# Kernel tuning notes

Measured on AMD Instinct MI355X. Metric: run time of the kernel, lower is better.

## Reference

```python
import jax, jax.numpy as jnp
import numpy as np

NEG = -9e15  # kept for fidelity though mask is unused in original forward

def setup_inputs() -> dict:
    key = jax.random.key(0)
    k1, k2, k3 = jax.random.split(key, 3)
    N, Fin, Fout = 8192, 512, 256
    x = jax.random.normal(k1, (N, Fin), dtype=jnp.float32)
    # xavier_uniform with gain=1.414 ~ U(-b, b), b = gain*sqrt(6/(fan_in+fan_out))
    bW = 1.414 * np.sqrt(6.0 / (Fin + Fout))
    W = jax.random.uniform(k2, (Fin, Fout), minval=-bW, maxval=bW, dtype=jnp.float32)
    ba = 1.414 * np.sqrt(6.0 / (2 * Fout + 1))
    a = jax.random.uniform(k3, (2 * Fout, 1), minval=-ba, maxval=ba, dtype=jnp.float32)
    return {"x": x, "W": W, "a": a}

def reference(x, W, a):
    # h: [N, Fout]
    h = x @ W
    Fout = h.shape[1]
    # Algebraic decomposition of additive score: e_ij = relu(a1.h_i + a2.h_j)
    a1, a2 = a[:Fout, 0], a[Fout:, 0]  # [Fout], [Fout]
    f = h @ a1  # [N] contribution of row node i
    g = h @ a2  # [N] contribution of col node j
    e = jax.nn.relu(f[:, None] + g[None, :])  # [N, N]
    attention = jax.nn.softmax(e, axis=1)
    h_prime = attention @ h  # [N, Fout]
    return jax.nn.elu(h_prime)
```

## Files before the change

### kernel.cpp

```cpp
#include <hip/hip_runtime.h>
#include <math.h>

#define NROWS 8192
#define FIN   512
#define FOUT  256
#define NCHUNK 512
#define CHROWS 16

typedef _Float16 f16;
typedef _Float16 f16x8 __attribute__((ext_vector_type(8)));
typedef float    f32x4 __attribute__((ext_vector_type(4)));

__global__ __launch_bounds__(256) void prep_wt(const float* __restrict__ W,
                                               f16* __restrict__ Wt,
                                               float* __restrict__ fg) {
    const int n = blockIdx.x, t = threadIdx.x;
    Wt[(size_t)n * FIN + t]       = (f16)W[(size_t)t * FOUT + n];
    Wt[(size_t)n * FIN + t + 256] = (f16)W[(size_t)(t + 256) * FOUT + n];
    if (n < 64) fg[n * 256 + t] = 0.f;
}

__global__ __launch_bounds__(256) void gemm_fg(const float* __restrict__ x,
                                               const f16* __restrict__ Wt,
                                               const float* __restrict__ a,
                                               f16* __restrict__ h,
                                               float* __restrict__ f,
                                               float* __restrict__ g) {
    __shared__ __align__(16) f16 As[64][136];
    __shared__ __align__(16) f16 Bs[64][136];
    __shared__ float sf[2][64], sg[2][64];
    const int tid = threadIdx.x;
    const int n0 = blockIdx.x * 64;
    const int m0 = blockIdx.y * 64;
    const int srow = tid >> 2, sseg = (tid & 3) * 8;
    const int w = tid >> 6, lane = tid & 63;
    const int wm = (w & 1) * 32, wn = (w >> 1) * 32;
    const int l15 = lane & 15, quad = lane >> 4;

    float4 pa0[4], pa1[4];
    f16x8 pb[4];
#pragma unroll
    for (int j = 0; j < 4; ++j) {
        const float* xp = &x[(size_t)(m0 + srow) * FIN + j * 32 + sseg];
        pa0[j] = *(const float4*)xp;
        pa1[j] = *(const float4*)(xp + 4);
        pb[j] = *(const f16x8*)&Wt[(size_t)(n0 + srow) * FIN + j * 32 + sseg];
    }

    f32x4 acc[2][2] = {};
    for (int k0 = 0; k0 < FIN; k0 += 128) {
        __syncthreads();
#pragma unroll
        for (int j = 0; j < 4; ++j) {
            f16x8 t;
            t[0] = (f16)pa0[j].x; t[1] = (f16)pa0[j].y;
            t[2] = (f16)pa0[j].z; t[3] = (f16)pa0[j].w;
            t[4] = (f16)pa1[j].x; t[5] = (f16)pa1[j].y;
            t[6] = (f16)pa1[j].z; t[7] = (f16)pa1[j].w;
            *(f16x8*)&As[srow][j * 32 + sseg] = t;
            *(f16x8*)&Bs[srow][j * 32 + sseg] = pb[j];
        }
        __syncthreads();
        if (k0 + 128 < FIN) {
#pragma unroll
            for (int j = 0; j < 4; ++j) {
                const float* xp = &x[(size_t)(m0 + srow) * FIN + k0 + 128 + j * 32 + sseg];
                pa0[j] = *(const float4*)xp;
                pa1[j] = *(const float4*)(xp + 4);
                pb[j] = *(const f16x8*)&Wt[(size_t)(n0 + srow) * FIN + k0 + 128 + j * 32 + sseg];
            }
        }
#pragma unroll
        for (int kk = 0; kk < 4; ++kk) {
            f16x8 af[2], bf[2];
#pragma unroll
            for (int ti = 0; ti < 2; ++ti)
                af[ti] = *(const f16x8*)&As[wm + ti * 16 + l15][kk * 32 + quad * 8];
#pragma unroll
            for (int tj = 0; tj < 2; ++tj)
                bf[tj] = *(const f16x8*)&Bs[wn + tj * 16 + l15][kk * 32 + quad * 8];
#pragma unroll
            for (int ti = 0; ti < 2; ++ti)
#pragma unroll
                for (int tj = 0; tj < 2; ++tj)
                    acc[ti][tj] = __builtin_amdgcn_mfma_f32_16x16x32_f16(af[ti], bf[tj], acc[ti][tj], 0, 0, 0);
        }
    }
#pragma unroll
    for (int ti = 0; ti < 2; ++ti)
#pragma unroll
        for (int tj = 0; tj < 2; ++tj) {
            const int col = n0 + wn + tj * 16 + l15;
#pragma unroll
            for (int r = 0; r < 4; ++r) {
                const int row = m0 + wm + ti * 16 + quad * 4 + r;
                h[(size_t)row * FOUT + col] = (f16)acc[ti][tj][r];
            }
        }
    const float a1c0 = a[n0 + wn + l15];
    const float a1c1 = a[n0 + wn + 16 + l15];
    const float a2c0 = a[FOUT + n0 + wn + l15];
    const float a2c1 = a[FOUT + n0 + wn + 16 + l15];
    const int wnIdx = w >> 1;
#pragma unroll
    for (int ti = 0; ti < 2; ++ti) {
        float pf[4], pg[4];
#pragma unroll
        for (int r = 0; r < 4; ++r) {
            pf[r] = acc[ti][0][r] * a1c0 + acc[ti][1][r] * a1c1;
            pg[r] = acc[ti][0][r] * a2c0 + acc[ti][1][r] * a2c1;
        }
#pragma unroll
        for (int off = 8; off >= 1; off >>= 1)
#pragma unroll
            for (int r = 0; r < 4; ++r) {
                pf[r] += __shfl_xor(pf[r], off, 16);
                pg[r] += __shfl_xor(pg[r], off, 16);
            }
        if (l15 == 0)
#pragma unroll
            for (int r = 0; r < 4; ++r) {
                sf[wnIdx][wm + ti * 16 + quad * 4 + r] = pf[r];
                sg[wnIdx][wm + ti * 16 + quad * 4 + r] = pg[r];
            }
    }
    __syncthreads();
    if (tid < 64) {
        atomicAdd(&f[m0 + tid], sf[0][tid] + sf[1][tid]);
        atomicAdd(&g[m0 + tid], sg[0][tid] + sg[1][tid]);
    }
}

__global__ __launch_bounds__(256) void rank_scatter(const float* __restrict__ g,
                                                    float* __restrict__ gs,
                                                    int* __restrict__ perm) {
    const int t = threadIdx.x;
    const int jl = t & 31;
    const int seg = t >> 5;
    const int j = blockIdx.x * 32 + jl;
    const float gj = g[j];
    const int base = seg * (NROWS / 8);
    int cnt = 0;
    for (int r = 0; r < NROWS / 8; r += 4) {
        const float4 v = *(const float4*)&g[base + r];
        const int i0 = base + r;
        cnt += (v.x < gj) || (v.x == gj && (i0 + 0) < j);
        cnt += (v.y < gj) || (v.y == gj && (i0 + 1) < j);
        cnt += (v.z < gj) || (v.z == gj && (i0 + 2) < j);
        cnt += (v.w < gj) || (v.w == gj && (i0 + 3) < j);
    }
    __shared__ int part[8][32];
    part[seg][jl] = cnt;
    __syncthreads();
    if (seg == 0) {
        int rank = 0;
#pragma unroll
        for (int s = 0; s < 8; ++s) rank += part[s][jl];
        gs[rank] = gj;
        perm[rank] = j;
    }
}

__global__ __launch_bounds__(256) void scan_pass1(const f16* __restrict__ h,
                                                  const int* __restrict__ perm,
                                                  const float* __restrict__ gs,
                                                  const float* __restrict__ f,
                                                  float* __restrict__ c0,
                                                  float* __restrict__ c1,
                                                  float* __restrict__ c1s,
                                                  int* __restrict__ n0arr) {
    const int b = blockIdx.x, c = threadIdx.x;
    if (b < NCHUNK) {
        const int base = b * CHROWS;
        __shared__ int p[CHROWS];
        __shared__ float wl[CHROWS];
        if (c < CHROWS) {
            p[c] = perm[base + c];
            wl[c] = expf(gs[base + c] - gs[NROWS - 1]);
        }
        __syncthreads();
        float s0 = 0.f, s1 = 0.f;
        for (int r = 0; r < CHROWS; ++r) {
            float v = (float)h[(size_t)p[r] * FOUT + c];
            s0 += v;
            s1 += wl[r] * v;
        }
        c0[b * FOUT + c] = s0;
        c1[b * FOUT + c] = s1;
        if (c == 0) {
            float t = 0.f;
            for (int r = 0; r < CHROWS; ++r) t += wl[r];
            c1s[b] = t;
        }
    } else {
        const int i = (b - NCHUNK) * 256 + c;
        const float tt = -f[i];
        int lo = 0, hi = NROWS;
        while (lo < hi) {
            int mid = (lo + hi) >> 1;
            if (gs[mid] <= tt) lo = mid + 1; else hi = mid;
        }
        n0arr[i] = lo;
    }
}

__global__ __launch_bounds__(256) void scan_pass2(const float* __restrict__ c0,
                                                  const float* __restrict__ c1,
                                                  const float* __restrict__ c1s,
                                                  float* __restrict__ o0,
                                                  float* __restrict__ o1,
                                                  float* __restrict__ o1s) {
    const int b = blockIdx.x, t = threadIdx.x;
    __shared__ float sb[256];
    if (b < 256) {
        const float e0 = c0[(2 * t) * FOUT + b];
        const float e1 = c0[(2 * t + 1) * FOUT + b];
        const float local = e0 + e1;
        sb[t] = local;
        __syncthreads();
        for (int off = 1; off < 256; off <<= 1) {
            float add = (t >= off) ? sb[t - off] : 0.f;
            __syncthreads();
            sb[t] += add;
            __syncthreads();
        }
        const float ex = sb[t] - local;
        o0[(2 * t) * FOUT + b] = ex;
        o0[(2 * t + 1) * FOUT + b] = ex + e0;
    } else if (b < 512) {
        const int col = b - 256;
        const float e0 = c1[(2 * t) * FOUT + col];
        const float e1 = c1[(2 * t + 1) * FOUT + col];
        const float local = e0 + e1;
        sb[t] = local;
        __syncthreads();
        for (int off = 1; off < 256; off <<= 1) {
            float add = (t + off < 256) ? sb[t + off] : 0.f;
            __syncthreads();
            sb[t] += add;
            __syncthreads();
        }
        const float exs = sb[t] - local;
        o1[(2 * t) * FOUT + col] = exs + e1;
        o1[(2 * t + 1) * FOUT + col] = exs;
    } else {
        const float e0 = c1s[2 * t];
        const float e1 = c1s[2 * t + 1];
        const float local = e0 + e1;
        sb[t] = local;
        __syncthreads();
        for (int off = 1; off < 256; off <<= 1) {
            float add = (t + off < 256) ? sb[t + off] : 0.f;
            __syncthreads();
            sb[t] += add;
            __syncthreads();
        }
        const float exs = sb[t] - local;
        o1s[2 * t] = exs + e1;
        o1s[2 * t + 1] = exs;
    }
}

__global__ __launch_bounds__(256) void scan_pass3(const f16* __restrict__ h,
                                                  const int* __restrict__ perm,
                                                  const float* __restrict__ gs,
                                                  const float* __restrict__ o0,
                                                  const float* __restrict__ o1,
                                                  const float* __restrict__ o1s,
                                                  f16* __restrict__ P0,
                                                  f16* __restrict__ S1,
                                                  float* __restrict__ S1s) {
    const int k = blockIdx.x, c = threadIdx.x;
    const int base = k * CHROWS;
    __shared__ int p[CHROWS];
    __shared__ float wl[CHROWS];
    if (c < CHROWS) {
        p[c] = perm[base + c];
        wl[c] = expf(gs[base + c] - gs[NROWS - 1]);
    }
    __syncthreads();
    float run0 = o0[k * FOUT + c];
    for (int r = 0; r < CHROWS; ++r) {
        P0[(size_t)(base + r) * FOUT + c] = (f16)run0;
        run0 += (float)h[(size_t)p[r] * FOUT + c];
    }
    float run1 = o1[k * FOUT + c];
    for (int r = CHROWS - 1; r >= 0; --r) {
        run1 += wl[r] * (float)h[(size_t)p[r] * FOUT + c];
        S1[(size_t)(base + r) * FOUT + c] = (f16)run1;
    }
    if (c == 0) {
        float rs = o1s[k];
        for (int r = CHROWS - 1; r >= 0; --r) { rs += wl[r]; S1s[base + r] = rs; }
    }
    if (k == NCHUNK - 1) {
        P0[(size_t)NROWS * FOUT + c] = (f16)run0;
        S1[(size_t)NROWS * FOUT + c] = (f16)0.f;
        if (c == 0) S1s[NROWS] = 0.f;
    }
}

__global__ __launch_bounds__(256) void final_kernel(const float* __restrict__ f,
                                                    const float* __restrict__ gs,
                                                    const int* __restrict__ n0arr,
                                                    const f16* __restrict__ P0,
                                                    const f16* __restrict__ S1,
                                                    const float* __restrict__ S1s,
                                                    float* __restrict__ out) {
    const int b = blockIdx.x, c = threadIdx.x;
    const float gm = gs[NROWS - 1];
#pragma unroll
    for (int rr = 0; rr < 4; ++rr) {
        const int i = b * 4 + rr;
        const float fi = f[i];
        const int n0 = n0arr[i];
        const float m = fmaxf(0.f, fi + gm);
        const float A = expf(-m);
        const float B = expf(fi + gm - m);
        const float denom = A * (float)n0 + B * S1s[n0];
        const float numer = A * (float)P0[(size_t)n0 * FOUT + c]
                          + B * (float)S1[(size_t)n0 * FOUT + c];
        const float v = numer / denom;
        out[(size_t)i * FOUT + c] = v > 0.f ? v : expm1f(v);
    }
}

extern "C" void kernel_launch(void* const* d_in, const int* in_sizes, int n_in,
                              void* d_out, int out_size, void* d_ws, size_t ws_size,
                              hipStream_t stream) {
    (void)in_sizes; (void)n_in; (void)out_size; (void)ws_size;
    const float* x = (const float*)d_in[0];
    const float* W = (const float*)d_in[1];
    const float* a = (const float*)d_in[2];
    float* out = (float*)d_out;

    char* ws = (char*)d_ws;
    size_t off = 0;
    auto alloc = [&](size_t bytes) -> void* {
        void* p = ws + off;
        off += (bytes + 255) & ~(size_t)255;
        return p;
    };
    f16*   Wt   = (f16*)alloc((size_t)FOUT * FIN * 2);
    f16*   h    = (f16*)alloc((size_t)NROWS * FOUT * 2);
    f16*   P0   = (f16*)alloc((size_t)(NROWS + 1) * FOUT * 2);
    f16*   S1   = (f16*)alloc((size_t)(NROWS + 1) * FOUT * 2);
    float* fg   = (float*)alloc(2 * NROWS * 4);
    float* f    = fg;
    float* g    = fg + NROWS;
    float* gs   = (float*)alloc(NROWS * 4);
    int*   perm = (int*)alloc(NROWS * 4);
    int*   n0arr= (int*)alloc(NROWS * 4);
    float* c0   = (float*)alloc(NCHUNK * FOUT * 4);
    float* c1   = (float*)alloc(NCHUNK * FOUT * 4);
    float* o0   = (float*)alloc(NCHUNK * FOUT * 4);
    float* o1   = (float*)alloc(NCHUNK * FOUT * 4);
    float* c1s  = (float*)alloc(NCHUNK * 4);
    float* o1s  = (float*)alloc(NCHUNK * 4);
    float* S1s  = (float*)alloc((NROWS + 1) * 4);

    prep_wt<<<256, 256, 0, stream>>>(W, Wt, fg);
    gemm_fg<<<dim3(FOUT / 64, NROWS / 64), 256, 0, stream>>>(x, Wt, a, h, f, g);
    rank_scatter<<<NROWS / 32, 256, 0, stream>>>(g, gs, perm);
    scan_pass1<<<NCHUNK + 32, 256, 0, stream>>>(h, perm, gs, f, c0, c1, c1s, n0arr);
    scan_pass2<<<513, 256, 0, stream>>>(c0, c1, c1s, o0, o1, o1s);
    scan_pass3<<<NCHUNK, 256, 0, stream>>>(h, perm, gs, o0, o1, o1s, P0, S1, S1s);
    final_kernel<<<NROWS / 4, 256, 0, stream>>>(f, gs, n0arr, P0, S1, S1s, out);
}
```

Before: 135.4 us.

## Widen GEMM tile to 64x128 with 512 threads and split rank counting finer

```diff
diff --git a/kernel.cpp b/kernel.cpp
--- a/kernel.cpp
+++ b/kernel.cpp
@@ -20,110 +20,108 @@
     if (n < 64) fg[n * 256 + t] = 0.f;
 }
 
-__global__ __launch_bounds__(256) void gemm_fg(const float* __restrict__ x,
+__global__ __launch_bounds__(512) void gemm_fg(const float* __restrict__ x,
                                                const f16* __restrict__ Wt,
                                                const float* __restrict__ a,
                                                f16* __restrict__ h,
                                                float* __restrict__ f,
                                                float* __restrict__ g) {
     __shared__ __align__(16) f16 As[64][136];
-    __shared__ __align__(16) f16 Bs[64][136];
+    __shared__ __align__(16) f16 Bs[128][136];
     __shared__ float sf[2][64], sg[2][64];
     const int tid = threadIdx.x;
-    const int n0 = blockIdx.x * 64;
+    const int n0 = blockIdx.x * 128;
     const int m0 = blockIdx.y * 64;
-    const int srow = tid >> 2, sseg = (tid & 3) * 8;
+    const int arow = tid >> 3, aseg = (tid & 7) * 16;
+    const int brow = tid >> 2, bseg = (tid & 3) * 32;
     const int w = tid >> 6, lane = tid & 63;
-    const int wm = (w & 1) * 32, wn = (w >> 1) * 32;
+    const int wm = (w & 3) * 16, wn = (w >> 2) * 64;
     const int l15 = lane & 15, quad = lane >> 4;
 
-    float4 pa0[4], pa1[4];
+    float4 pa[4];
     f16x8 pb[4];
 #pragma unroll
     for (int j = 0; j < 4; ++j) {
-        const float* xp = &x[(size_t)(m0 + srow) * FIN + j * 32 + sseg];
-        pa0[j] = *(const float4*)xp;
-        pa1[j] = *(const float4*)(xp + 4);
-        pb[j] = *(const f16x8*)&Wt[(size_t)(n0 + srow) * FIN + j * 32 + sseg];
-    }
-
-    f32x4 acc[2][2] = {};
+        pa[j] = *(const float4*)&x[(size_t)(m0 + arow) * FIN + aseg + j * 4];
+        pb[j] = *(const f16x8*)&Wt[(size_t)(n0 + brow) * FIN + bseg + j * 8];
+    }
+
+    f32x4 acc[4] = {};
     for (int k0 = 0; k0 < FIN; k0 += 128) {
         __syncthreads();
-#pragma unroll
-        for (int j = 0; j < 4; ++j) {
-            f16x8 t;
-            t[0] = (f16)pa0[j].x; t[1] = (f16)pa0[j].y;
-            t[2] = (f16)pa0[j].z; t[3] = (f16)pa0[j].w;
-            t[4] = (f16)pa1[j].x; t[5] = (f16)pa1[j].y;
-            t[6] = (f16)pa1[j].z; t[7] = (f16)pa1[j].w;
-            *(f16x8*)&As[srow][j * 32 + sseg] = t;
-            *(f16x8*)&Bs[srow][j * 32 + sseg] = pb[j];
-        }
+        {
+            f16x8 t0, t1;
+            t0[0] = (f16)pa[0].x; t0[1] = (f16)pa[0].y;
+            t0[2] = (f16)pa[0].z; t0[3] = (f16)pa[0].w;
+            t0[4] = (f16)pa[1].x; t0[5] = (f16)pa[1].y;
+            t0[6] = (f16)pa[1].z; t0[7] = (f16)pa[1].w;
+            t1[0] = (f16)pa[2].x; t1[1] = (f16)pa[2].y;
+            t1[2] = (f16)pa[2].z; t1[3] = (f16)pa[2].w;
+            t1[4] = (f16)pa[3].x; t1[5] = (f16)pa[3].y;
+            t1[6] = (f16)pa[3].z; t1[7] = (f16)pa[3].w;
+            *(f16x8*)&As[arow][aseg]     = t0;
+            *(f16x8*)&As[arow][aseg + 8] = t1;
+        }
+#pragma unroll
+        for (int j = 0; j < 4; ++j)
+            *(f16x8*)&Bs[brow][bseg + j * 8] = pb[j];
         __syncthreads();
         if (k0 + 128 < FIN) {
 #pragma unroll
             for (int j = 0; j < 4; ++j) {
-                const float* xp = &x[(size_t)(m0 + srow) * FIN + k0 + 128 + j * 32 + sseg];
-                pa0[j] = *(const float4*)xp;
-                pa1[j] = *(const float4*)(xp + 4);
-                pb[j] = *(const f16x8*)&Wt[(size_t)(n0 + srow) * FIN + k0 + 128 + j * 32 + sseg];
+                pa[j] = *(const float4*)&x[(size_t)(m0 + arow) * FIN + k0 + 128 + aseg + j * 4];
+                pb[j] = *(const f16x8*)&Wt[(size_t)(n0 + brow) * FIN + k0 + 128 + bseg + j * 8];
             }
         }
 #pragma unroll
         for (int kk = 0; kk < 4; ++kk) {
-            f16x8 af[2], bf[2];
-#pragma unroll
-            for (int ti = 0; ti < 2; ++ti)
-                af[ti] = *(const f16x8*)&As[wm + ti * 16 + l15][kk * 32 + quad * 8];
-#pragma unroll
-            for (int tj = 0; tj < 2; ++tj)
+            const f16x8 af = *(const f16x8*)&As[wm + l15][kk * 32 + quad * 8];
+            f16x8 bf[4];
+#pragma unroll
+            for (int tj = 0; tj < 4; ++tj)
                 bf[tj] = *(const f16x8*)&Bs[wn + tj * 16 + l15][kk * 32 + quad * 8];
 #pragma unroll
-            for (int ti = 0; ti < 2; ++ti)
-#pragma unroll
-                for (int tj = 0; tj < 2; ++tj)
-                    acc[ti][tj] = __builtin_amdgcn_mfma_f32_16x16x32_f16(af[ti], bf[tj], acc[ti][tj], 0, 0, 0);
-        }
-    }
-#pragma unroll
-    for (int ti = 0; ti < 2; ++ti)
-#pragma unroll
-        for (int tj = 0; tj < 2; ++tj) {
-            const int col = n0 + wn + tj * 16 + l15;
-#pragma unroll
-            for (int r = 0; r < 4; ++r) {
-                const int row = m0 + wm + ti * 16 + quad * 4 + r;
-                h[(size_t)row * FOUT + col] = (f16)acc[ti][tj][r];
-            }
-        }
-    const float a1c0 = a[n0 + wn + l15];
-    const float a1c1 = a[n0 + wn + 16 + l15];
-    const float a2c0 = a[FOUT + n0 + wn + l15];
-    const float a2c1 = a[FOUT + n0 + wn + 16 + l15];
-    const int wnIdx = w >> 1;
-#pragma unroll
-    for (int ti = 0; ti < 2; ++ti) {
-        float pf[4], pg[4];
+            for (int tj = 0; tj < 4; ++tj)
+                acc[tj] = __builtin_amdgcn_mfma_f32_16x16x32_f16(af, bf[tj], acc[tj], 0, 0, 0);
+        }
+    }
+#pragma unroll
+    for (int tj = 0; tj < 4; ++tj) {
+        const int col = n0 + wn + tj * 16 + l15;
 #pragma unroll
         for (int r = 0; r < 4; ++r) {
-            pf[r] = acc[ti][0][r] * a1c0 + acc[ti][1][r] * a1c1;
-            pg[r] = acc[ti][0][r] * a2c0 + acc[ti][1][r] * a2c1;
-        }
-#pragma unroll
-        for (int off = 8; off >= 1; off >>= 1)
-#pragma unroll
-            for (int r = 0; r < 4; ++r) {
-                pf[r] += __shfl_xor(pf[r], off, 16);
-                pg[r] += __shfl_xor(pg[r], off, 16);
-            }
-        if (l15 == 0)
-#pragma unroll
-            for (int r = 0; r < 4; ++r) {
-                sf[wnIdx][wm + ti * 16 + quad * 4 + r] = pf[r];
-                sg[wnIdx][wm + ti * 16 + quad * 4 + r] = pg[r];
-            }
-    }
+            const int row = m0 + wm + quad * 4 + r;
+            h[(size_t)row * FOUT + col] = (f16)acc[tj][r];
+        }
+    }
+    float a1c[4], a2c[4];
+#pragma unroll
+    for (int tj = 0; tj < 4; ++tj) {
+        a1c[tj] = a[n0 + wn + tj * 16 + l15];
+        a2c[tj] = a[FOUT + n0 + wn + tj * 16 + l15];
+    }
+    float pf[4], pg[4];
+#pragma unroll
+    for (int r = 0; r < 4; ++r) {
+        pf[r] = acc[0][r] * a1c[0] + acc[1][r] * a1c[1]
+              + acc[2][r] * a1c[2] + acc[3][r] * a1c[3];
+        pg[r] = acc[0][r] * a2c[0] + acc[1][r] * a2c[1]
+              + acc[2][r] * a2c[2] + acc[3][r] * a2c[3];
+    }
+#pragma unroll
+    for (int off = 8; off >= 1; off >>= 1)
+#pragma unroll
+        for (int r = 0; r < 4; ++r) {
+            pf[r] += __shfl_xor(pf[r], off, 16);
+            pg[r] += __shfl_xor(pg[r], off, 16);
+        }
+    const int ng = w >> 2;
+    if (l15 == 0)
+#pragma unroll
+        for (int r = 0; r < 4; ++r) {
+            sf[ng][wm + quad * 4 + r] = pf[r];
+            sg[ng][wm + quad * 4 + r] = pg[r];
+        }
     __syncthreads();
     if (tid < 64) {
         atomicAdd(&f[m0 + tid], sf[0][tid] + sf[1][tid]);
@@ -135,13 +133,14 @@
                                                     float* __restrict__ gs,
                                                     int* __restrict__ perm) {
     const int t = threadIdx.x;
-    const int jl = t & 31;
-    const int seg = t >> 5;
-    const int j = blockIdx.x * 32 + jl;
+    const int jl = t & 15;
+    const int seg = t >> 4;
+    const int j = blockIdx.x * 16 + jl;
     const float gj = g[j];
-    const int base = seg * (NROWS / 8);
+    const int base = seg * 512;
     int cnt = 0;
-    for (int r = 0; r < NROWS / 8; r += 4) {
+#pragma unroll 4
+    for (int r = 0; r < 512; r += 4) {
         const float4 v = *(const float4*)&g[base + r];
         const int i0 = base + r;
         cnt += (v.x < gj) || (v.x == gj && (i0 + 0) < j);
@@ -149,13 +148,13 @@
         cnt += (v.z < gj) || (v.z == gj && (i0 + 2) < j);
         cnt += (v.w < gj) || (v.w == gj && (i0 + 3) < j);
     }
-    __shared__ int part[8][32];
+    __shared__ int part[16][16];
     part[seg][jl] = cnt;
     __syncthreads();
     if (seg == 0) {
         int rank = 0;
 #pragma unroll
-        for (int s = 0; s < 8; ++s) rank += part[s][jl];
+        for (int ss = 0; ss < 16; ++ss) rank += part[ss][jl];
         gs[rank] = gj;
         perm[rank] = j;
     }
@@ -360,8 +359,8 @@
     float* S1s  = (float*)alloc((NROWS + 1) * 4);
 
     prep_wt<<<256, 256, 0, stream>>>(W, Wt, fg);
-    gemm_fg<<<dim3(FOUT / 64, NROWS / 64), 256, 0, stream>>>(x, Wt, a, h, f, g);
-    rank_scatter<<<NROWS / 32, 256, 0, stream>>>(g, gs, perm);
+    gemm_fg<<<dim3(FOUT / 128, NROWS / 64), 512, 0, stream>>>(x, Wt, a, h, f, g);
+    rank_scatter<<<NROWS / 16, 256, 0, stream>>>(g, gs, perm);
     scan_pass1<<<NCHUNK + 32, 256, 0, stream>>>(h, perm, gs, f, c0, c1, c1s, n0arr);
     scan_pass2<<<513, 256, 0, stream>>>(c0, c1, c1s, o0, o1, o1s);
     scan_pass3<<<NCHUNK, 256, 0, stream>>>(h, perm, gs, o0, o1, o1s, P0, S1, S1s);
```

Result: faster. 117.6 us (median of 2 runs) (-13.2%).
